# Kernel tuning notes

Measured on AMD Instinct MI355X. Metric: run time of the kernel, lower is better.

## Reference

```python
import jax, jax.numpy as jnp
import numpy as np

J = 1.0          # coupling constant
PT_PERIOD = 4    # parallel-tempering exchange every PT_PERIOD sweeps


def setup_inputs() -> dict:
    key = jax.random.key(0)
    k1, k2 = jax.random.split(key)
    B, C, L = 32, 16, 256
    # temperatures across the Ising critical region, sorted ascending
    T = jnp.sort(1.5 + 2.0 * jax.random.uniform(k1, (B,), dtype=jnp.float32))
    # spins stored as {0,1} ints; converted to +/-1 inside reference
    spins = jax.random.randint(k2, (B, C, L, L), 0, 2).astype(jnp.int32)
    return {"T": T, "spins": spins, "n_sweeps": 16}


def _neighbor_sum(s):
    # periodic 4-neighbor sum, shape preserved [B,C,L,L]
    return (jnp.roll(s, 1, -1) + jnp.roll(s, -1, -1)
            + jnp.roll(s, 1, -2) + jnp.roll(s, -1, -2))


def _energy(s):
    # total Ising energy per chain: -J * sum_<ij> s_i s_j  -> [B, C]
    return -J * jnp.sum(s * (jnp.roll(s, -1, -1) + jnp.roll(s, -1, -2)), axis=(-1, -2))


def reference(T, spins, n_sweeps):
    B, C, L, _ = spins.shape
    s = spins.astype(jnp.float32) * 2.0 - 1.0          # +/-1 spins
    ii = jnp.arange(L)
    parity = (ii[:, None] + ii[None, :]) % 2            # [L,L] checkerboard
    Tb = T[:, None, None, None]                         # [B,1,1,1]
    beta = 1.0 / T                                      # [B]
    base_key = jax.random.key(42)

    def half_sweep(s, key, color):
        dE = 2.0 * J * s * _neighbor_sum(s)             # local energy change on flip
        u = jax.random.uniform(key, s.shape, dtype=jnp.float32)
        acc = u < jnp.exp(-dE / Tb)                     # Metropolis accept
        mask = (parity == color)                        # update one sub-lattice only
        return jnp.where(mask & acc, -s, s)

    def pt_swap(s, key, pair_parity):
        # attempt swaps between adjacent temperatures (b, b+1) with given pair parity
        E = _energy(s)                                  # [B, C]
        d = (beta[:-1] - beta[1:])[:, None] * (E[:-1] - E[1:])   # [B-1, C]
        u = jax.random.uniform(key, (B - 1, C), dtype=jnp.float32)
        pair_mask = (jnp.arange(B - 1) % 2) == pair_parity
        acc = (u < jnp.exp(d)) & pair_mask[:, None]     # [B-1, C] non-overlapping
        swap_next = jnp.concatenate([acc, jnp.zeros((1, C), bool)], 0)  # swap b<->b+1
        swap_prev = jnp.concatenate([jnp.zeros((1, C), bool), acc], 0)
        s_next = jnp.roll(s, -1, axis=0)
        s_prev = jnp.roll(s, 1, axis=0)
        swn = swap_next[:, :, None, None]
        swp = swap_prev[:, :, None, None]
        return jnp.where(swn, s_next, jnp.where(swp, s_prev, s))

    def sweep(s, t):
        kb = jax.random.fold_in(base_key, t)
        k1, k2, k3 = jax.random.split(kb, 3)
        s = half_sweep(s, k1, 0)   # black sub-lattice
        s = half_sweep(s, k2, 1)   # white sub-lattice
        do_pt = (t % PT_PERIOD) == (PT_PERIOD - 1)
        s = jax.lax.cond(do_pt,
                         lambda s_: pt_swap(s_, k3, (t // PT_PERIOD) % 2),
                         lambda s_: s_, s)
        return s, None

    s, _ = jax.lax.scan(sweep, s, jnp.arange(n_sweeps))
    return s, _energy(s)
```

## Files before the change

### kernel.cpp

```cpp
#include <hip/hip_runtime.h>
#include <stdint.h>


#define BB 32
#define CC 16
#define PLANE 65536
#define NSITE (BB * CC * PLANE)
#define NPAIR ((BB - 1) * CC)
#define HSTRIP 32
#define ROWS_LD (HSTRIP + 4)

__host__ __device__ __forceinline__ void tf2x32(uint32_t k0, uint32_t k1,
                                                uint32_t c0, uint32_t c1,
                                                uint32_t& o0, uint32_t& o1) {
  uint32_t ks2 = k0 ^ k1 ^ 0x1BD11BDAu;
  uint32_t x0 = c0 + k0;
  uint32_t x1 = c1 + k1;
#define TF_ROT(r) { x0 += x1; x1 = (x1 << (r)) | (x1 >> (32 - (r))); x1 ^= x0; }
  TF_ROT(13) TF_ROT(15) TF_ROT(26) TF_ROT(6)
  x0 += k1;  x1 += ks2 + 1u;
  TF_ROT(17) TF_ROT(29) TF_ROT(16) TF_ROT(24)
  x0 += ks2; x1 += k0 + 2u;
  TF_ROT(13) TF_ROT(15) TF_ROT(26) TF_ROT(6)
  x0 += k0;  x1 += k1 + 3u;
  TF_ROT(17) TF_ROT(29) TF_ROT(16) TF_ROT(24)
  x0 += k1;  x1 += ks2 + 4u;
  TF_ROT(13) TF_ROT(15) TF_ROT(26) TF_ROT(6)
  x0 += ks2; x1 += k0 + 5u;
#undef TF_ROT
  o0 = x0; o1 = x1;
}

__device__ __forceinline__ float u01(uint32_t bits) {
  return __uint_as_float((bits >> 9) | 0x3f800000u) - 1.0f;
}

__global__ __launch_bounds__(256) void init8_k(const int* __restrict__ spins,
                                               int8_t* __restrict__ s) {
  int i = blockIdx.x * 256 + threadIdx.x;
  int4 v = ((const int4*)spins)[i];
  uchar4 o;
  o.x = (uint8_t)(int8_t)(2 * v.x - 1);
  o.y = (uint8_t)(int8_t)(2 * v.y - 1);
  o.z = (uint8_t)(int8_t)(2 * v.z - 1);
  o.w = (uint8_t)(int8_t)(2 * v.w - 1);
  ((uchar4*)s)[i] = o;
}

__global__ void prep_k(const float* __restrict__ T,
                       float* __restrict__ thr4, float* __restrict__ thr8) {
  int b = threadIdx.x;
  if (b < BB) {
    float t = T[b];
    thr4[b] = (float)exp((double)((-4.0f) / t));
    thr8[b] = (float)exp((double)((-8.0f) / t));
  }
}

__global__ __launch_bounds__(256) void sweep_k(
    const int8_t* __restrict__ src, int8_t* __restrict__ dst,
    const float* __restrict__ thr4, const float* __restrict__ thr8,
    uint32_t kA0, uint32_t kA1, uint32_t kB0, uint32_t kB1,
    int t, const int* __restrict__ nsw) {
  __shared__ __align__(16) int8_t tile[ROWS_LD * 256];

  int bc    = blockIdx.x >> 3;
  int strip = blockIdx.x & 7;
  int y0    = strip * HSTRIP;
  int b     = bc >> 4;
  uint32_t bcbase = (uint32_t)bc << 16;
  const int8_t* sp = src + ((size_t)bc << 16);
  int8_t*       dp = dst + ((size_t)bc << 16);
  int tid = threadIdx.x;
  bool active = (t < *nsw);
  float t4 = thr4[b], t8 = thr8[b];

  for (int it = 0; it < 3; ++it) {
    int i = it * 256 + tid;
    if (i < ROWS_LD * 16) {
      int gy = (y0 - 2 + (i >> 4)) & 255;
      ((uint4*)tile)[i] = *(const uint4*)(sp + (gy << 8) + ((i & 15) << 4));
    }
  }
  __syncthreads();

  if (active) {
    int tq = tid >> 7;
    int k  = tid & 127;

    for (int it = 0; it < 17; ++it) {
      int j  = 1 + it * 2 + tq;
      int gy = (y0 - 2 + j) & 255;
      int x  = (k << 1) | (gy & 1);
      int8_t sv = tile[j * 256 + x];
      int nsum = (int)tile[j * 256 + ((x + 1) & 255)]
               + (int)tile[j * 256 + ((x + 255) & 255)]
               + (int)tile[(j - 1) * 256 + x]
               + (int)tile[(j + 1) * 256 + x];
      int prod = (int)sv * nsum;
      bool acc = true;
      if (prod > 0) {
        uint32_t h0, h1;
        tf2x32(kA0, kA1, 0u, bcbase + ((uint32_t)gy << 8) + (uint32_t)x, h0, h1);
        float u = u01(h0 ^ h1);
        acc = u < (prod == 2 ? t4 : t8);
      }
      if (acc) tile[j * 256 + x] = (int8_t)(-sv);
    }
    __syncthreads();

    for (int it = 0; it < 16; ++it) {
      int j  = 2 + it * 2 + tq;
      int gy = (y0 - 2 + j) & 255;
      int x  = (k << 1) | ((gy + 1) & 1);
      int8_t sv = tile[j * 256 + x];
      int nsum = (int)tile[j * 256 + ((x + 1) & 255)]
               + (int)tile[j * 256 + ((x + 255) & 255)]
               + (int)tile[(j - 1) * 256 + x]
               + (int)tile[(j + 1) * 256 + x];
      int prod = (int)sv * nsum;
      bool acc = true;
      if (prod > 0) {
        uint32_t h0, h1;
        tf2x32(kB0, kB1, 0u, bcbase + ((uint32_t)gy << 8) + (uint32_t)x, h0, h1);
        float u = u01(h0 ^ h1);
        acc = u < (prod == 2 ? t4 : t8);
      }
      if (acc) tile[j * 256 + x] = (int8_t)(-sv);
    }
  }
  __syncthreads();

  for (int it = 0; it < 2; ++it) {
    int i = it * 256 + tid;
    int gy = y0 + (i >> 4);
    *(uint4*)(dp + (gy << 8) + ((i & 15) << 4)) = ((uint4*)tile)[32 + i];
  }
}

__global__ __launch_bounds__(256) void energy8_k(const int8_t* __restrict__ s,
                                                 float* __restrict__ Edst) {
  int bc = blockIdx.x;
  const uint8_t* p = (const uint8_t*)(s + ((size_t)bc << 16));
  int tid = threadIdx.x;
  int xg = tid & 63;
  int acc = 0;
  for (int i = 0; i < 64; ++i) {
    int y  = (tid >> 6) + i * 4;
    int y1 = (y + 1) & 255;
    uint32_t cur = *(const uint32_t*)(p + (y << 8) + (xg << 2));
    uint32_t nxt = *(const uint32_t*)(p + (y << 8) + (((xg + 1) & 63) << 2));
    uint32_t dwn = *(const uint32_t*)(p + (y1 << 8) + (xg << 2));
    uint32_t rsh = (cur >> 8) | (nxt << 24);
    int d1 = __builtin_popcount((cur ^ rsh) & 0x02020202u);
    int d2 = __builtin_popcount((cur ^ dwn) & 0x02020202u);
    acc += 8 - 2 * (d1 + d2);
  }
  int lane = tid & 63, wid = tid >> 6;
  for (int off = 32; off > 0; off >>= 1) acc += __shfl_down(acc, off, 64);
  __shared__ int red[4];
  if (lane == 0) red[wid] = acc;
  __syncthreads();
  if (tid == 0) Edst[bc] = -(float)(red[0] + red[1] + red[2] + red[3]);
}

__global__ void pt_decide_k(const float* __restrict__ E,
                            const float* __restrict__ T,
                            uint32_t k0, uint32_t k1, int pair_parity,
                            int* __restrict__ accf, int t,
                            const int* __restrict__ nsw) {
  int tid = threadIdx.x;
  if (tid >= NPAIR) return;
  if (t >= *nsw) { accf[tid] = 0; return; }
  int b = tid >> 4;
  float beta_b  = 1.0f / T[b];
  float beta_b1 = 1.0f / T[b + 1];
  float d = (beta_b - beta_b1) * (E[tid] - E[tid + CC]);
  uint32_t h0, h1;
  tf2x32(k0, k1, 0u, (uint32_t)tid, h0, h1);
  float u = u01(h0 ^ h1);
  float th = (float)exp((double)d);
  accf[tid] = (u < th) && ((b & 1) == pair_parity);
}

__global__ __launch_bounds__(256) void pt_swap8_k(int8_t* __restrict__ s,
                                                  const int* __restrict__ accf) {
  int pc = blockIdx.x;
  if (!accf[pc]) return;
  uint4* p0 = (uint4*)(s + ((size_t)pc << 16));
  uint4* p1 = p0 + (CC * PLANE / 16);
  for (int j = threadIdx.x; j < PLANE / 16; j += 256) {
    uint4 a0 = p0[j], a1 = p1[j];
    p0[j] = a1; p1[j] = a0;
  }
}

__global__ __launch_bounds__(256) void expand_k(const int8_t* __restrict__ st,
                                                float* __restrict__ out,
                                                int lo, int cnt4) {
  int i = blockIdx.x * 256 + threadIdx.x;
  if (i >= cnt4) return;
  uint32_t v = *(const uint32_t*)(st + lo + 4 * i);
  float4 o;
  o.x = (float)(int8_t)(v);
  o.y = (float)(int8_t)(v >> 8);
  o.z = (float)(int8_t)(v >> 16);
  o.w = (float)(int8_t)(v >> 24);
  ((float4*)out)[(lo >> 2) + i] = o;
}

__global__ __launch_bounds__(256) void expand_head_k(const int8_t* __restrict__ st,
                                                     float* __restrict__ out) {
  uint32_t r[8];
  int t = threadIdx.x;
  for (int u = 0; u < 8; ++u) r[u] = *(const uint32_t*)(st + t * 32 + 4 * u);
  __syncthreads();
  for (int u = 0; u < 8; ++u) {
    uint32_t v = r[u];
    float4 o;
    o.x = (float)(int8_t)(v);
    o.y = (float)(int8_t)(v >> 8);
    o.z = (float)(int8_t)(v >> 16);
    o.w = (float)(int8_t)(v >> 24);
    ((float4*)out)[t * 8 + u] = o;
  }
}

extern "C" void kernel_launch(void* const* d_in, const int* in_sizes, int n_in,
                              void* d_out, int out_size, void* d_ws, size_t ws_size,
                              hipStream_t stream) {
  (void)in_sizes; (void)n_in; (void)out_size; (void)ws_size;
  const float* T    = (const float*)d_in[0];
  const int*  spins = (const int*)d_in[1];
  const int*  nsw   = (const int*)d_in[2];

  int8_t* buf0 = (int8_t*)d_out;
  int8_t* buf1 = buf0 + NSITE;
  float*  outf = (float*)d_out;
  float*  Eout = outf + NSITE;

  float* Eplane = (float*)d_ws;
  float* thr4   = Eplane + BB * CC;
  float* thr8   = thr4 + BB;
  int*   accf   = (int*)(thr8 + BB);

  init8_k<<<NSITE / 1024, 256, 0, stream>>>(spins, buf0);
  prep_k<<<1, 64, 0, stream>>>(T, thr4, thr8);

  for (int t = 0; t < 16; ++t) {
    uint32_t kb0, kb1;
    tf2x32(0u, 42u, 0u, (uint32_t)t, kb0, kb1);
    uint32_t k1a, k1b, k2a, k2b, k3a, k3b;
    tf2x32(kb0, kb1, 0u, 0u, k1a, k1b);
    tf2x32(kb0, kb1, 0u, 1u, k2a, k2b);
    tf2x32(kb0, kb1, 0u, 2u, k3a, k3b);

    int8_t* src = (t & 1) ? buf1 : buf0;
    int8_t* dst = (t & 1) ? buf0 : buf1;
    sweep_k<<<BB * CC * 8, 256, 0, stream>>>(src, dst, thr4, thr8,
                                             k1a, k1b, k2a, k2b, t, nsw);
    if ((t & 3) == 3) {
      energy8_k<<<BB * CC, 256, 0, stream>>>(buf0, Eplane);
      pt_decide_k<<<1, 512, 0, stream>>>(Eplane, T, k3a, k3b, (t >> 2) & 1,
                                         accf, t, nsw);
      pt_swap8_k<<<NPAIR, 256, 0, stream>>>(buf0, accf);
    }
  }

  energy8_k<<<BB * CC, 256, 0, stream>>>(buf0, Eout);

  for (int lo = NSITE / 4; lo >= 8192; lo >>= 2) {
    int cnt4 = (lo * 3) / 4;
    expand_k<<<(cnt4 + 255) / 256, 256, 0, stream>>>(buf0, outf, lo, cnt4);
  }
  expand_head_k<<<1, 256, 0, stream>>>(buf0, outf);
}
```

Baseline: 1.563 ms.

## Fuse energy into sweep, pack spins per word, widen strips, integer thresholds

The sweep kernel now processes four packed spins per 32-bit word. Each lane computes neighbour counts with byte-wise bit tricks and compares integer mantissa bits against precomputed integer thresholds, replacing the float compare. Strips grow from 32 to 64 rows, which halves the block count and the halo reload overhead. The per-plane energy needed for parallel tempering is computed from the shared tile inside the sweep, as per-strip partial sums reduced in pt_decide, so the separate energy pass is removed. The final energy is derived from the last PT step's energies permuted by the swap decisions. This risks correctness if the final sweep is not the PT sweep or if n_sweeps differs from 16.

```diff
diff --git a/kernel.cpp b/kernel.cpp
--- a/kernel.cpp
+++ b/kernel.cpp
@@ -7,8 +7,8 @@
 #define PLANE 65536
 #define NSITE (BB * CC * PLANE)
 #define NPAIR ((BB - 1) * CC)
-#define HSTRIP 32
-#define ROWS_LD (HSTRIP + 4)
+#define HSTRIP 64
+#define ROWS_LD 69
 
 __host__ __device__ __forceinline__ void tf2x32(uint32_t k0, uint32_t k1,
                                                 uint32_t c0, uint32_t c1,
@@ -36,154 +36,155 @@
 }
 
 __global__ __launch_bounds__(256) void init8_k(const int* __restrict__ spins,
-                                               int8_t* __restrict__ s) {
+                                               uint8_t* __restrict__ s) {
   int i = blockIdx.x * 256 + threadIdx.x;
   int4 v = ((const int4*)spins)[i];
-  uchar4 o;
-  o.x = (uint8_t)(int8_t)(2 * v.x - 1);
-  o.y = (uint8_t)(int8_t)(2 * v.y - 1);
-  o.z = (uint8_t)(int8_t)(2 * v.z - 1);
-  o.w = (uint8_t)(int8_t)(2 * v.w - 1);
-  ((uchar4*)s)[i] = o;
+  uint32_t o = ((uint32_t)(uint8_t)(int8_t)(2 * v.x - 1))
+             | ((uint32_t)(uint8_t)(int8_t)(2 * v.y - 1) << 8)
+             | ((uint32_t)(uint8_t)(int8_t)(2 * v.z - 1) << 16)
+             | ((uint32_t)(uint8_t)(int8_t)(2 * v.w - 1) << 24);
+  ((uint32_t*)s)[i] = o;
 }
 
 __global__ void prep_k(const float* __restrict__ T,
-                       float* __restrict__ thr4, float* __restrict__ thr8) {
+                       uint32_t* __restrict__ M4, uint32_t* __restrict__ M8) {
   int b = threadIdx.x;
   if (b < BB) {
     float t = T[b];
-    thr4[b] = (float)exp((double)((-4.0f) / t));
-    thr8[b] = (float)exp((double)((-8.0f) / t));
-  }
+    float th4 = (float)exp((double)((-4.0f) / t));
+    float th8 = (float)exp((double)((-8.0f) / t));
+    M4[b] = (uint32_t)ceil((double)th4 * 8388608.0);
+    M8[b] = (uint32_t)ceil((double)th8 * 8388608.0);
+  }
+}
+
+__device__ __forceinline__ void process_row(uint32_t* tile32, int j, int y0,
+                                            int lane, uint32_t bcbase,
+                                            int color, uint32_t k0, uint32_t k1,
+                                            uint32_t M4b, uint32_t M8b) {
+  int gy = (y0 - 2 + j) & 255;
+  uint32_t rowkey = bcbase + ((uint32_t)gy << 8) + (uint32_t)(lane << 2);
+  int base = j * 64 + lane;
+  uint32_t cur = tile32[base];
+  uint32_t up  = tile32[base - 64];
+  uint32_t dn  = tile32[base + 64];
+  uint32_t pw  = tile32[j * 64 + ((lane + 63) & 63)];
+  uint32_t nw  = tile32[j * 64 + ((lane + 1) & 63)];
+  uint32_t lft = (cur << 8) | (pw >> 24);
+  uint32_t rgt = (cur >> 8) | (nw << 24);
+  uint32_t kd = ((up >> 1) & 0x01010101u) + ((dn >> 1) & 0x01010101u)
+              + ((lft >> 1) & 0x01010101u) + ((rgt >> 1) & 0x01010101u);
+  int p = (gy + color) & 1;
+  uint32_t flip = 0;
+#pragma unroll
+  for (int sIt = 0; sIt < 2; ++sIt) {
+    int i = p + 2 * sIt;
+    uint32_t kdi = (kd >> (8 * i)) & 0xFFu;
+    uint32_t si  = (cur >> (8 * i + 1)) & 1u;
+    uint32_t m   = si ? (4u - kdi) : kdi;
+    bool accept = true;
+    if (m < 2u) {
+      uint32_t h0, h1;
+      tf2x32(k0, k1, 0u, rowkey + (uint32_t)i, h0, h1);
+      uint32_t n = (h0 ^ h1) >> 9;
+      accept = n < (m == 1u ? M4b : M8b);
+    }
+    if (accept) flip |= (0xFEu << (8 * i));
+  }
+  tile32[base] = cur ^ flip;
 }
 
 __global__ __launch_bounds__(256) void sweep_k(
-    const int8_t* __restrict__ src, int8_t* __restrict__ dst,
-    const float* __restrict__ thr4, const float* __restrict__ thr8,
+    const uint8_t* __restrict__ src, uint8_t* __restrict__ dst,
+    const uint32_t* __restrict__ M4, const uint32_t* __restrict__ M8,
     uint32_t kA0, uint32_t kA1, uint32_t kB0, uint32_t kB1,
-    int t, const int* __restrict__ nsw) {
-  __shared__ __align__(16) int8_t tile[ROWS_LD * 256];
-
-  int bc    = blockIdx.x >> 3;
-  int strip = blockIdx.x & 7;
-  int y0    = strip * HSTRIP;
+    int t, const int* __restrict__ nsw, float* __restrict__ Estrip, int doE) {
+  __shared__ __align__(16) uint32_t tile32[ROWS_LD * 64];
+  __shared__ int red[4];
+  int tid   = threadIdx.x;
+  int bc    = blockIdx.x >> 2;
+  int strip = blockIdx.x & 3;
+  int y0    = strip << 6;
   int b     = bc >> 4;
   uint32_t bcbase = (uint32_t)bc << 16;
-  const int8_t* sp = src + ((size_t)bc << 16);
-  int8_t*       dp = dst + ((size_t)bc << 16);
-  int tid = threadIdx.x;
+  const uint8_t* sp = src + ((size_t)bc << 16);
+  uint8_t*       dp = dst + ((size_t)bc << 16);
   bool active = (t < *nsw);
-  float t4 = thr4[b], t8 = thr8[b];
-
-  for (int it = 0; it < 3; ++it) {
+  uint32_t M4b = M4[b], M8b = M8[b];
+
+  for (int it = 0; it < 5; ++it) {
     int i = it * 256 + tid;
     if (i < ROWS_LD * 16) {
       int gy = (y0 - 2 + (i >> 4)) & 255;
-      ((uint4*)tile)[i] = *(const uint4*)(sp + (gy << 8) + ((i & 15) << 4));
-    }
-  }
-  __syncthreads();
+      ((uint4*)tile32)[i] = *(const uint4*)(sp + (gy << 8) + ((i & 15) << 4));
+    }
+  }
+  __syncthreads();
+
+  int w = tid >> 6, lane = tid & 63;
 
   if (active) {
-    int tq = tid >> 7;
-    int k  = tid & 127;
-
-    for (int it = 0; it < 17; ++it) {
-      int j  = 1 + it * 2 + tq;
-      int gy = (y0 - 2 + j) & 255;
-      int x  = (k << 1) | (gy & 1);
-      int8_t sv = tile[j * 256 + x];
-      int nsum = (int)tile[j * 256 + ((x + 1) & 255)]
-               + (int)tile[j * 256 + ((x + 255) & 255)]
-               + (int)tile[(j - 1) * 256 + x]
-               + (int)tile[(j + 1) * 256 + x];
-      int prod = (int)sv * nsum;
-      bool acc = true;
-      if (prod > 0) {
-        uint32_t h0, h1;
-        tf2x32(kA0, kA1, 0u, bcbase + ((uint32_t)gy << 8) + (uint32_t)x, h0, h1);
-        float u = u01(h0 ^ h1);
-        acc = u < (prod == 2 ? t4 : t8);
-      }
-      if (acc) tile[j * 256 + x] = (int8_t)(-sv);
-    }
-    __syncthreads();
-
-    for (int it = 0; it < 16; ++it) {
-      int j  = 2 + it * 2 + tq;
-      int gy = (y0 - 2 + j) & 255;
-      int x  = (k << 1) | ((gy + 1) & 1);
-      int8_t sv = tile[j * 256 + x];
-      int nsum = (int)tile[j * 256 + ((x + 1) & 255)]
-               + (int)tile[j * 256 + ((x + 255) & 255)]
-               + (int)tile[(j - 1) * 256 + x]
-               + (int)tile[(j + 1) * 256 + x];
-      int prod = (int)sv * nsum;
-      bool acc = true;
-      if (prod > 0) {
-        uint32_t h0, h1;
-        tf2x32(kB0, kB1, 0u, bcbase + ((uint32_t)gy << 8) + (uint32_t)x, h0, h1);
-        float u = u01(h0 ^ h1);
-        acc = u < (prod == 2 ? t4 : t8);
-      }
-      if (acc) tile[j * 256 + x] = (int8_t)(-sv);
-    }
-  }
-  __syncthreads();
-
-  for (int it = 0; it < 2; ++it) {
+    for (int j = 1 + w; j < 68; j += 4)
+      process_row(tile32, j, y0, lane, bcbase, 0, kA0, kA1, M4b, M8b);
+  }
+  __syncthreads();
+  if (active) {
+    for (int j = 2 + w; j < 67; j += 4)
+      process_row(tile32, j, y0, lane, bcbase, 1, kB0, kB1, M4b, M8b);
+  }
+  __syncthreads();
+
+  for (int it = 0; it < 4; ++it) {
     int i = it * 256 + tid;
     int gy = y0 + (i >> 4);
-    *(uint4*)(dp + (gy << 8) + ((i & 15) << 4)) = ((uint4*)tile)[32 + i];
-  }
-}
-
-__global__ __launch_bounds__(256) void energy8_k(const int8_t* __restrict__ s,
-                                                 float* __restrict__ Edst) {
-  int bc = blockIdx.x;
-  const uint8_t* p = (const uint8_t*)(s + ((size_t)bc << 16));
-  int tid = threadIdx.x;
-  int xg = tid & 63;
-  int acc = 0;
-  for (int i = 0; i < 64; ++i) {
-    int y  = (tid >> 6) + i * 4;
-    int y1 = (y + 1) & 255;
-    uint32_t cur = *(const uint32_t*)(p + (y << 8) + (xg << 2));
-    uint32_t nxt = *(const uint32_t*)(p + (y << 8) + (((xg + 1) & 63) << 2));
-    uint32_t dwn = *(const uint32_t*)(p + (y1 << 8) + (xg << 2));
-    uint32_t rsh = (cur >> 8) | (nxt << 24);
-    int d1 = __builtin_popcount((cur ^ rsh) & 0x02020202u);
-    int d2 = __builtin_popcount((cur ^ dwn) & 0x02020202u);
-    acc += 8 - 2 * (d1 + d2);
-  }
-  int lane = tid & 63, wid = tid >> 6;
-  for (int off = 32; off > 0; off >>= 1) acc += __shfl_down(acc, off, 64);
-  __shared__ int red[4];
-  if (lane == 0) red[wid] = acc;
-  __syncthreads();
-  if (tid == 0) Edst[bc] = -(float)(red[0] + red[1] + red[2] + red[3]);
-}
-
-__global__ void pt_decide_k(const float* __restrict__ E,
+    *(uint4*)(dp + (gy << 8) + ((i & 15) << 4)) = ((uint4*)tile32)[32 + i];
+  }
+
+  if (doE) {
+    int acc = 0;
+#pragma unroll 4
+    for (int q = 0; q < 16; ++q) {
+      int j = 2 + w + 4 * q;
+      uint32_t cur = tile32[j * 64 + lane];
+      uint32_t nxt = tile32[j * 64 + ((lane + 1) & 63)];
+      uint32_t dwn = tile32[j * 64 + 64 + lane];
+      uint32_t rsh = (cur >> 8) | (nxt << 24);
+      int d = __builtin_popcount((cur ^ rsh) & 0x02020202u)
+            + __builtin_popcount((cur ^ dwn) & 0x02020202u);
+      acc += 8 - 2 * d;
+    }
+    for (int off = 32; off > 0; off >>= 1) acc += __shfl_down(acc, off, 64);
+    if (lane == 0) red[w] = acc;
+    __syncthreads();
+    if (tid == 0)
+      Estrip[blockIdx.x] = (float)(red[0] + red[1] + red[2] + red[3]);
+  }
+}
+
+__global__ void pt_decide_k(const float* __restrict__ Estrip,
                             const float* __restrict__ T,
+                            float* __restrict__ Eplane,
                             uint32_t k0, uint32_t k1, int pair_parity,
                             int* __restrict__ accf, int t,
                             const int* __restrict__ nsw) {
   int tid = threadIdx.x;
-  if (tid >= NPAIR) return;
-  if (t >= *nsw) { accf[tid] = 0; return; }
-  int b = tid >> 4;
-  float beta_b  = 1.0f / T[b];
-  float beta_b1 = 1.0f / T[b + 1];
-  float d = (beta_b - beta_b1) * (E[tid] - E[tid + CC]);
-  uint32_t h0, h1;
-  tf2x32(k0, k1, 0u, (uint32_t)tid, h0, h1);
-  float u = u01(h0 ^ h1);
-  float th = (float)exp((double)d);
-  accf[tid] = (u < th) && ((b & 1) == pair_parity);
-}
-
-__global__ __launch_bounds__(256) void pt_swap8_k(int8_t* __restrict__ s,
+  float e = Estrip[tid * 4] + Estrip[tid * 4 + 1]
+          + Estrip[tid * 4 + 2] + Estrip[tid * 4 + 3];
+  Eplane[tid] = -e;
+  __syncthreads();
+  if (tid < NPAIR) {
+    if (t >= *nsw) { accf[tid] = 0; return; }
+    int b = tid >> 4;
+    float d = (1.0f / T[b] - 1.0f / T[b + 1]) * (Eplane[tid] - Eplane[tid + 16]);
+    uint32_t h0, h1;
+    tf2x32(k0, k1, 0u, (uint32_t)tid, h0, h1);
+    float u = u01(h0 ^ h1);
+    float th = (float)exp((double)d);
+    accf[tid] = (u < th) && ((b & 1) == pair_parity);
+  }
+}
+
+__global__ __launch_bounds__(256) void pt_swap8_k(uint8_t* __restrict__ s,
                                                   const int* __restrict__ accf) {
   int pc = blockIdx.x;
   if (!accf[pc]) return;
@@ -193,6 +194,17 @@
     uint4 a0 = p0[j], a1 = p1[j];
     p0[j] = a1; p1[j] = a0;
   }
+}
+
+__global__ void final_eout_k(const float* __restrict__ Eplane,
+                             const int* __restrict__ accf,
+                             float* __restrict__ Eout) {
+  int tid = threadIdx.x;
+  int b = tid >> 4;
+  float e = Eplane[tid];
+  if (b < 31 && accf[tid])      e = Eplane[tid + 16];
+  if (b > 0  && accf[tid - 16]) e = Eplane[tid - 16];
+  Eout[tid] = e;
 }
 
 __global__ __launch_bounds__(256) void expand_k(const int8_t* __restrict__ st,
@@ -234,18 +246,19 @@
   const int*  spins = (const int*)d_in[1];
   const int*  nsw   = (const int*)d_in[2];
 
-  int8_t* buf0 = (int8_t*)d_out;
-  int8_t* buf1 = buf0 + NSITE;
-  float*  outf = (float*)d_out;
-  float*  Eout = outf + NSITE;
-
-  float* Eplane = (float*)d_ws;
-  float* thr4   = Eplane + BB * CC;
-  float* thr8   = thr4 + BB;
-  int*   accf   = (int*)(thr8 + BB);
+  uint8_t* buf0 = (uint8_t*)d_out;
+  uint8_t* buf1 = buf0 + NSITE;
+  float*   outf = (float*)d_out;
+  float*   Eout = outf + NSITE;
+
+  float*    Estrip = (float*)d_ws;
+  float*    Eplane = Estrip + 2048;
+  uint32_t* M4     = (uint32_t*)(Eplane + 512);
+  uint32_t* M8     = M4 + BB;
+  int*      accf   = (int*)(M8 + BB);
 
   init8_k<<<NSITE / 1024, 256, 0, stream>>>(spins, buf0);
-  prep_k<<<1, 64, 0, stream>>>(T, thr4, thr8);
+  prep_k<<<1, 64, 0, stream>>>(T, M4, M8);
 
   for (int t = 0; t < 16; ++t) {
     uint32_t kb0, kb1;
@@ -255,23 +268,24 @@
     tf2x32(kb0, kb1, 0u, 1u, k2a, k2b);
     tf2x32(kb0, kb1, 0u, 2u, k3a, k3b);
 
-    int8_t* src = (t & 1) ? buf1 : buf0;
-    int8_t* dst = (t & 1) ? buf0 : buf1;
-    sweep_k<<<BB * CC * 8, 256, 0, stream>>>(src, dst, thr4, thr8,
-                                             k1a, k1b, k2a, k2b, t, nsw);
-    if ((t & 3) == 3) {
-      energy8_k<<<BB * CC, 256, 0, stream>>>(buf0, Eplane);
-      pt_decide_k<<<1, 512, 0, stream>>>(Eplane, T, k3a, k3b, (t >> 2) & 1,
-                                         accf, t, nsw);
+    uint8_t* src = (t & 1) ? buf1 : buf0;
+    uint8_t* dst = (t & 1) ? buf0 : buf1;
+    int doE = ((t & 3) == 3);
+    sweep_k<<<BB * CC * 4, 256, 0, stream>>>(src, dst, M4, M8,
+                                             k1a, k1b, k2a, k2b, t, nsw,
+                                             Estrip, doE);
+    if (doE) {
+      pt_decide_k<<<1, 512, 0, stream>>>(Estrip, T, Eplane, k3a, k3b,
+                                         (t >> 2) & 1, accf, t, nsw);
       pt_swap8_k<<<NPAIR, 256, 0, stream>>>(buf0, accf);
     }
   }
 
-  energy8_k<<<BB * CC, 256, 0, stream>>>(buf0, Eout);
+  final_eout_k<<<1, 512, 0, stream>>>(Eplane, accf, Eout);
 
   for (int lo = NSITE / 4; lo >= 8192; lo >>= 2) {
     int cnt4 = (lo * 3) / 4;
-    expand_k<<<(cnt4 + 255) / 256, 256, 0, stream>>>(buf0, outf, lo, cnt4);
-  }
-  expand_head_k<<<1, 256, 0, stream>>>(buf0, outf);
-}
+    expand_k<<<(cnt4 + 255) / 256, 256, 0, stream>>>((int8_t*)buf0, outf, lo, cnt4);
+  }
+  expand_head_k<<<1, 256, 0, stream>>>((int8_t*)buf0, outf);
+}
```

Measured after the change: 1.676 ms. 7.2% more time.
